# Performance work log

Measured on AMD Instinct MI355X. Metric: run time of the kernel, lower is better.

The kernel has to match this reference:

```python
import jax, jax.numpy as jnp
import numpy as np

K = 3  # s_kernel_size = max_graph_distance + 1

def setup_inputs() -> dict:
    key = jax.random.key(0)
    k1, k2, k3, k4, k5 = jax.random.split(key, 5)
    N, C_IN, T, V = 64, 64, 300, 25
    C_OUT = 128
    x = jax.random.normal(k1, (N, C_IN, T, V), dtype=jnp.float32)
    A = jax.random.uniform(k2, (K, V, V), dtype=jnp.float32)
    # 1x1 Conv2d(in=64, out=128*3) -> weight [384, 64] (kernel dims squeezed), bias [384]
    weight = jax.random.normal(k3, (C_OUT * K, C_IN), dtype=jnp.float32) * 0.05
    bias = jax.random.normal(k4, (C_OUT * K,), dtype=jnp.float32) * 0.05
    index = jax.random.randint(k5, (V,), 0, V, dtype=jnp.int64)
    return {"x": x, "A": A, "weight": weight, "bias": bias, "index": index}

def reference(x, A, weight, bias, index):
    n, c_in, t, v = x.shape
    kc = weight.shape[0]
    c_out = kc // K
    # 1x1 conv == channel GEMM: [n, kc, t, v]
    y = jnp.einsum('nitv,oi->notv', x, weight) + bias[None, :, None, None]
    # split kernel dim: [n, K, c_out, t, v]
    y = y.reshape(n, K, c_out, t, v)
    # gather adjacency rows: A[:K, index, :] -> [K, v, w]
    A_sel = A[:K, index, :]
    # contract over k and w (v shared between y and A_sel)
    out = jnp.einsum('nkctv,kvw->nctv', y, A_sel)
    return out
```

## Files before the change

### kernel.cpp

```cpp
#include <hip/hip_runtime.h>
#include <cstddef>
#include <cstdint>

#define N_DIM 64
#define C_IN 64
#define C_OUT 128
#define T_DIM 300
#define V_DIM 25
#define TVTOT (T_DIM * V_DIM)
#define TILE 64
#define NTILE ((TVTOT + TILE - 1) / TILE)
#define KTOT 192
#define NKS (KTOT / 32)
#define ROWB 384
#define WFRAG_BYTES (8 * NKS * 64 * 8 * 2)
#define SS4_OFF WFRAG_BYTES
#define BEFF_OFF (WFRAG_BYTES + 1024)

typedef unsigned int uint32;
typedef unsigned short ushort16;
typedef float f32x4 __attribute__((ext_vector_type(4)));
typedef short bf16x8 __attribute__((ext_vector_type(8)));
typedef uint32 u32x4 __attribute__((ext_vector_type(4)));

__device__ __forceinline__ ushort16 f2bf(float f) {
  uint32 u = __float_as_uint(f);
  u = (u + 0x7FFFu + ((u >> 16) & 1u)) >> 16;
  return (ushort16)u;
}
__device__ __forceinline__ uint32 pack2(float a, float b) {
  return (uint32)f2bf(a) | ((uint32)f2bf(b) << 16);
}
__device__ __forceinline__ uint32 cvt_pk(float lo, float hi) {
  uint32 r;
  asm("v_cvt_pk_bf16_f32 %0, %1, %2" : "=v"(r) : "v"(lo), "v"(hi));
  return r;
}

__global__ __launch_bounds__(384)
void sgc_prep(const float* __restrict__ A, const float* __restrict__ W,
              const float* __restrict__ bias, const int* __restrict__ index,
              ushort16* __restrict__ Wfrag, float* __restrict__ sS4,
              float* __restrict__ beff) {
  __shared__ float sl[3 * V_DIM];
  const int m = blockIdx.x;
  const int tid = threadIdx.x;

  if (m == 0) {
    if (tid < 3 * V_DIM) {
      const int k = tid / V_DIM;
      const int v = tid - k * V_DIM;
      const int idx = index[v];
      float s = 0.f;
      #pragma unroll
      for (int w = 0; w < V_DIM; ++w) s += A[(k * V_DIM + idx) * V_DIM + w];
      sl[k * V_DIM + v] = s;
      sS4[v * 4 + k] = s;
      if (k == 0) sS4[v * 4 + 3] = 0.f;
    }
    __syncthreads();
    if (tid < C_OUT) {
      const float b0 = bias[tid];
      const float b1 = bias[C_OUT + tid];
      const float b2 = bias[2 * C_OUT + tid];
      #pragma unroll
      for (int v = 0; v < V_DIM; ++v)
        beff[v * C_OUT + tid] =
            sl[v] * b0 + sl[V_DIM + v] * b1 + sl[2 * V_DIM + v] * b2;
    }
  }

  const int ks = tid >> 6;
  const int lane = tid & 63;
  const int c = (m << 4) + (lane & 15);
  const int kk0 = (ks << 5) + ((lane >> 4) << 3);
  const int k = kk0 >> 6;
  const int i0 = kk0 & 63;
  const float* wrow = W + (size_t)(k * C_OUT + c) * C_IN + i0;
  u32x4 w4;
  #pragma unroll
  for (int p = 0; p < 4; ++p)
    w4[p] = pack2(wrow[2 * p], wrow[2 * p + 1]);
  *(u32x4*)((ushort16*)Wfrag + (((m * NKS + ks) * 64 + lane) << 3)) = w4;
}

__global__ __launch_bounds__(256)
void sgc_main(const float* __restrict__ x, const ushort16* __restrict__ Wfrag,
              const float* __restrict__ sS4, const float* __restrict__ beff,
              float* __restrict__ out) {
  __shared__ __align__(16) ushort16 xs[TILE * (ROWB / 2)];

  const int tid = threadIdx.x;
  const int wv = tid >> 6;
  const int lane = tid & 63;
  const int tile = blockIdx.x;
  const int n = blockIdx.y;
  const int tv0 = tile * TILE;

  bf16x8 afr[2][NKS];
  #pragma unroll
  for (int m2 = 0; m2 < 2; ++m2)
    #pragma unroll
    for (int ks = 0; ks < NKS; ++ks)
      afr[m2][ks] = *(const bf16x8*)((const ushort16*)Wfrag +
                        ((((2 * wv + m2) * NKS + ks) * 64 + lane) << 3));

  const int tvg = tv0 + lane;
  const bool tvok = tvg < TVTOT;
  const int vstage = tvok ? (tvg % V_DIM) : 0;
  const f32x4 sv = *(const f32x4*)(sS4 + 4 * vstage);
  float xv[16];
  {
    const float* xp = x + ((size_t)n * C_IN + wv * 16) * TVTOT + tvg;
    if (tvok) {
      #pragma unroll
      for (int j = 0; j < 16; ++j) xv[j] = xp[j * TVTOT];
    } else {
      #pragma unroll
      for (int j = 0; j < 16; ++j) xv[j] = 0.f;
    }
  }
  #pragma unroll
  for (int k = 0; k < 3; ++k) {
    const float sk = sv[k];
    u32x4 w0, w1;
    #pragma unroll
    for (int p = 0; p < 4; ++p) {
      w0[p] = cvt_pk(xv[2 * p] * sk, xv[2 * p + 1] * sk);
      w1[p] = cvt_pk(xv[8 + 2 * p] * sk, xv[9 + 2 * p] * sk);
    }
    const int sb = k * 8 + 2 * wv;
    char* rowp = (char*)xs + lane * ROWB;
    *(u32x4*)(rowp + ((sb ^ (lane & 7)) << 4)) = w0;
    *(u32x4*)(rowp + (((sb + 1) ^ (lane & 7)) << 4)) = w1;
  }
  __syncthreads();

  f32x4 acc[2][4];
  #pragma unroll
  for (int m2 = 0; m2 < 2; ++m2)
    #pragma unroll
    for (int f = 0; f < 4; ++f) acc[m2][f] = (f32x4){0.f, 0.f, 0.f, 0.f};

  #pragma unroll
  for (int ks = 0; ks < NKS; ++ks) {
    bf16x8 bfr[4];
    #pragma unroll
    for (int f = 0; f < 4; ++f) {
      const int col = 16 * f + (lane & 15);
      const int sl_ = (4 * ks + (lane >> 4)) ^ (lane & 7);
      bfr[f] = *(const bf16x8*)((const char*)xs + col * ROWB + (sl_ << 4));
    }
    #pragma unroll
    for (int m2 = 0; m2 < 2; ++m2)
      #pragma unroll
      for (int f = 0; f < 4; ++f)
        acc[m2][f] = __builtin_amdgcn_mfma_f32_16x16x32_bf16(
            bfr[f], afr[m2][ks], acc[m2][f], 0, 0, 0);
  }

  const int g4 = (lane >> 4) << 2;
  const int cl = lane & 15;
  float* outn = out + (size_t)n * C_OUT * TVTOT;
  #pragma unroll
  for (int f = 0; f < 4; ++f) {
    const int tvc = tv0 + 16 * f + g4;
    if (tvc < TVTOT) {
      const int vb = tvc % V_DIM;
      #pragma unroll
      for (int m2 = 0; m2 < 2; ++m2) {
        const int c = 32 * wv + 16 * m2 + cl;
        const float* bef = beff + c;
        f32x4 r;
        int v = vb;
        #pragma unroll
        for (int q = 0; q < 4; ++q) {
          r[q] = acc[m2][f][q] + bef[v * C_OUT];
          v = (v + 1 == V_DIM) ? 0 : v + 1;
        }
        *(f32x4*)(outn + (size_t)c * TVTOT + tvc) = r;
      }
    }
  }
}

extern "C" void kernel_launch(void* const* d_in, const int* in_sizes, int n_in,
                              void* d_out, int out_size, void* d_ws, size_t ws_size,
                              hipStream_t stream) {
  const float* x      = (const float*)d_in[0];
  const float* A      = (const float*)d_in[1];
  const float* weight = (const float*)d_in[2];
  const float* bias   = (const float*)d_in[3];
  const int*   index  = (const int*)d_in[4];
  float* out = (float*)d_out;

  ushort16* Wfrag = (ushort16*)d_ws;
  float* sS4  = (float*)((char*)d_ws + SS4_OFF);
  float* beff = (float*)((char*)d_ws + BEFF_OFF);

  sgc_prep<<<dim3(8), dim3(384), 0, stream>>>(A, weight, bias, index, Wfrag, sS4, beff);
  sgc_main<<<dim3(NTILE, N_DIM), dim3(256), 0, stream>>>(x, Wfrag, sS4, beff, out);
}
```

Before: 392.8 us.

## Process two batch samples per block to amortize weight fragment loads

Each block now handles batch indices n and n+32 together. It issues both samples' x loads up front, stages both into a doubled LDS buffer, then runs the MFMA GEMM and epilogue for each half while reusing the same register-resident weight fragments. This halves the grid and the per-block weight-fragment loads and gives more loads in flight per thread. In exchange it doubles LDS use and x register use, which may lower occupancy.

```diff
diff --git a/kernel.cpp b/kernel.cpp
--- a/kernel.cpp
+++ b/kernel.cpp
@@ -10,9 +10,11 @@
 #define TVTOT (T_DIM * V_DIM)
 #define TILE 64
 #define NTILE ((TVTOT + TILE - 1) / TILE)
+#define NHALF 32
 #define KTOT 192
 #define NKS (KTOT / 32)
 #define ROWB 384
+#define LDS_HALF (TILE * (ROWB / 2))
 #define WFRAG_BYTES (8 * NKS * 64 * 8 * 2)
 #define SS4_OFF WFRAG_BYTES
 #define BEFF_OFF (WFRAG_BYTES + 1024)
@@ -88,7 +90,7 @@
 void sgc_main(const float* __restrict__ x, const ushort16* __restrict__ Wfrag,
               const float* __restrict__ sS4, const float* __restrict__ beff,
               float* __restrict__ out) {
-  __shared__ __align__(16) ushort16 xs[TILE * (ROWB / 2)];
+  __shared__ __align__(16) ushort16 xs[2 * LDS_HALF];
 
   const int tid = threadIdx.x;
   const int wv = tid >> 6;
@@ -97,6 +99,25 @@
   const int n = blockIdx.y;
   const int tv0 = tile * TILE;
 
+  const int tvg = tv0 + lane;
+  const bool tvok = tvg < TVTOT;
+  const int vstage = tvok ? (tvg % V_DIM) : 0;
+
+  float xa[16], xb[16];
+  {
+    const float* xpA = x + ((size_t)n * C_IN + wv * 16) * TVTOT + tvg;
+    const float* xpB = xpA + (size_t)NHALF * C_IN * TVTOT;
+    if (tvok) {
+      #pragma unroll
+      for (int j = 0; j < 16; ++j) xa[j] = xpA[j * TVTOT];
+      #pragma unroll
+      for (int j = 0; j < 16; ++j) xb[j] = xpB[j * TVTOT];
+    } else {
+      #pragma unroll
+      for (int j = 0; j < 16; ++j) { xa[j] = 0.f; xb[j] = 0.f; }
+    }
+  }
+
   bf16x8 afr[2][NKS];
   #pragma unroll
   for (int m2 = 0; m2 < 2; ++m2)
@@ -105,80 +126,75 @@
       afr[m2][ks] = *(const bf16x8*)((const ushort16*)Wfrag +
                         ((((2 * wv + m2) * NKS + ks) * 64 + lane) << 3));
 
-  const int tvg = tv0 + lane;
-  const bool tvok = tvg < TVTOT;
-  const int vstage = tvok ? (tvg % V_DIM) : 0;
   const f32x4 sv = *(const f32x4*)(sS4 + 4 * vstage);
-  float xv[16];
-  {
-    const float* xp = x + ((size_t)n * C_IN + wv * 16) * TVTOT + tvg;
-    if (tvok) {
-      #pragma unroll
-      for (int j = 0; j < 16; ++j) xv[j] = xp[j * TVTOT];
-    } else {
-      #pragma unroll
-      for (int j = 0; j < 16; ++j) xv[j] = 0.f;
-    }
-  }
-  #pragma unroll
-  for (int k = 0; k < 3; ++k) {
-    const float sk = sv[k];
-    u32x4 w0, w1;
-    #pragma unroll
-    for (int p = 0; p < 4; ++p) {
-      w0[p] = cvt_pk(xv[2 * p] * sk, xv[2 * p + 1] * sk);
-      w1[p] = cvt_pk(xv[8 + 2 * p] * sk, xv[9 + 2 * p] * sk);
-    }
-    const int sb = k * 8 + 2 * wv;
-    char* rowp = (char*)xs + lane * ROWB;
-    *(u32x4*)(rowp + ((sb ^ (lane & 7)) << 4)) = w0;
-    *(u32x4*)(rowp + (((sb + 1) ^ (lane & 7)) << 4)) = w1;
+
+  #pragma unroll
+  for (int half = 0; half < 2; ++half) {
+    const float* xv = half ? xb : xa;
+    char* rowp = (char*)xs + half * (LDS_HALF * 2) + lane * ROWB;
+    #pragma unroll
+    for (int k = 0; k < 3; ++k) {
+      const float sk = sv[k];
+      u32x4 w0, w1;
+      #pragma unroll
+      for (int p = 0; p < 4; ++p) {
+        w0[p] = cvt_pk(xv[2 * p] * sk, xv[2 * p + 1] * sk);
+        w1[p] = cvt_pk(xv[8 + 2 * p] * sk, xv[9 + 2 * p] * sk);
+      }
+      const int sb = k * 8 + 2 * wv;
+      *(u32x4*)(rowp + ((sb ^ (lane & 7)) << 4)) = w0;
+      *(u32x4*)(rowp + (((sb + 1) ^ (lane & 7)) << 4)) = w1;
+    }
   }
   __syncthreads();
-
-  f32x4 acc[2][4];
-  #pragma unroll
-  for (int m2 = 0; m2 < 2; ++m2)
-    #pragma unroll
-    for (int f = 0; f < 4; ++f) acc[m2][f] = (f32x4){0.f, 0.f, 0.f, 0.f};
-
-  #pragma unroll
-  for (int ks = 0; ks < NKS; ++ks) {
-    bf16x8 bfr[4];
-    #pragma unroll
-    for (int f = 0; f < 4; ++f) {
-      const int col = 16 * f + (lane & 15);
-      const int sl_ = (4 * ks + (lane >> 4)) ^ (lane & 7);
-      bfr[f] = *(const bf16x8*)((const char*)xs + col * ROWB + (sl_ << 4));
-    }
-    #pragma unroll
-    for (int m2 = 0; m2 < 2; ++m2)
-      #pragma unroll
-      for (int f = 0; f < 4; ++f)
-        acc[m2][f] = __builtin_amdgcn_mfma_f32_16x16x32_bf16(
-            bfr[f], afr[m2][ks], acc[m2][f], 0, 0, 0);
-  }
 
   const int g4 = (lane >> 4) << 2;
   const int cl = lane & 15;
-  float* outn = out + (size_t)n * C_OUT * TVTOT;
-  #pragma unroll
-  for (int f = 0; f < 4; ++f) {
-    const int tvc = tv0 + 16 * f + g4;
-    if (tvc < TVTOT) {
-      const int vb = tvc % V_DIM;
-      #pragma unroll
-      for (int m2 = 0; m2 < 2; ++m2) {
-        const int c = 32 * wv + 16 * m2 + cl;
-        const float* bef = beff + c;
-        f32x4 r;
-        int v = vb;
+  #pragma unroll
+  for (int half = 0; half < 2; ++half) {
+    const char* base = (const char*)xs + half * (LDS_HALF * 2);
+    f32x4 acc[2][4];
+    #pragma unroll
+    for (int m2 = 0; m2 < 2; ++m2)
+      #pragma unroll
+      for (int f = 0; f < 4; ++f) acc[m2][f] = (f32x4){0.f, 0.f, 0.f, 0.f};
+
+    #pragma unroll
+    for (int ks = 0; ks < NKS; ++ks) {
+      bf16x8 bfr[4];
+      #pragma unroll
+      for (int f = 0; f < 4; ++f) {
+        const int col = 16 * f + (lane & 15);
+        const int sl_ = (4 * ks + (lane >> 4)) ^ (lane & 7);
+        bfr[f] = *(const bf16x8*)(base + col * ROWB + (sl_ << 4));
+      }
+      #pragma unroll
+      for (int m2 = 0; m2 < 2; ++m2)
         #pragma unroll
-        for (int q = 0; q < 4; ++q) {
-          r[q] = acc[m2][f][q] + bef[v * C_OUT];
-          v = (v + 1 == V_DIM) ? 0 : v + 1;
+        for (int f = 0; f < 4; ++f)
+          acc[m2][f] = __builtin_amdgcn_mfma_f32_16x16x32_bf16(
+              bfr[f], afr[m2][ks], acc[m2][f], 0, 0, 0);
+    }
+
+    float* outn = out + (size_t)(n + half * NHALF) * C_OUT * TVTOT;
+    #pragma unroll
+    for (int f = 0; f < 4; ++f) {
+      const int tvc = tv0 + 16 * f + g4;
+      if (tvc < TVTOT) {
+        const int vb = tvc % V_DIM;
+        #pragma unroll
+        for (int m2 = 0; m2 < 2; ++m2) {
+          const int c = 32 * wv + 16 * m2 + cl;
+          const float* bef = beff + c;
+          f32x4 r;
+          int v = vb;
+          #pragma unroll
+          for (int q = 0; q < 4; ++q) {
+            r[q] = acc[m2][f][q] + bef[v * C_OUT];
+            v = (v + 1 == V_DIM) ? 0 : v + 1;
+          }
+          *(f32x4*)(outn + (size_t)c * TVTOT + tvc) = r;
         }
-        *(f32x4*)(outn + (size_t)c * TVTOT + tvc) = r;
       }
     }
   }
@@ -199,5 +215,5 @@
   float* beff = (float*)((char*)d_ws + BEFF_OFF);
 
   sgc_prep<<<dim3(8), dim3(384), 0, stream>>>(A, weight, bias, index, Wfrag, sS4, beff);
-  sgc_main<<<dim3(NTILE, N_DIM), dim3(256), 0, stream>>>(x, Wfrag, sS4, beff, out);
-}
+  sgc_main<<<dim3(NTILE, NHALF), dim3(256), 0, stream>>>(x, Wfrag, sS4, beff, out);
+}
```

Measured after the change: 398.9 us. No clear change (+1.5%).
